# Kernel tuning notes

Measured on AMD Instinct MI355X. Metric: run time of the kernel, lower is better.

## Reference

```python
import jax, jax.numpy as jnp
import numpy as np

N_NODES, N_EDGES, N_EVAL = 100000, 1600000, 200000
IN_C, HID_C, OUT_C = 128, 256, 128


def setup_inputs() -> dict:
    key = jax.random.key(0)
    ks = jax.random.split(key, 10)
    x = jax.random.normal(ks[0], (N_NODES, IN_C), dtype=jnp.float32)
    edge_index = jax.random.randint(ks[1], (2, N_EDGES), 0, N_NODES)
    pos_edge_index = jax.random.randint(ks[2], (2, N_EVAL), 0, N_NODES)
    neg_edge_index = jax.random.randint(ks[3], (2, N_EVAL), 0, N_NODES)

    def glorot(k, fi, fo):
        return jax.random.normal(k, (fi, fo), dtype=jnp.float32) * np.float32(1.0 / np.sqrt(fi))

    W1 = glorot(ks[4], IN_C, HID_C); b1 = jnp.zeros((HID_C,), jnp.float32)
    W2 = glorot(ks[5], HID_C, HID_C); b2 = jnp.zeros((HID_C,), jnp.float32)
    W3 = glorot(ks[6], HID_C, OUT_C); b3 = jnp.zeros((OUT_C,), jnp.float32)
    return dict(x=x, edge_index=edge_index, pos_edge_index=pos_edge_index,
                neg_edge_index=neg_edge_index, W1=W1, b1=b1, W2=W2, b2=b2, W3=W3, b3=b3)


def gcn_layer(x, W, b, src, dst, deg_inv_sqrt):
    # GCNConv: D^{-1/2} (A + I) D^{-1/2} X W + b, degrees include self-loops.
    h = x @ W                                            # [N, F_out]
    norm = deg_inv_sqrt[src] * deg_inv_sqrt[dst]         # [E]
    msg = h[src] * norm[:, None]                          # [E, F_out] gathered messages
    agg = jax.ops.segment_sum(msg, dst, num_segments=x.shape[0])
    agg = agg + h * (deg_inv_sqrt * deg_inv_sqrt)[:, None]  # self-loop contribution
    return agg + b


def reference(x, edge_index, pos_edge_index, neg_edge_index, W1, b1, W2, b2, W3, b3):
    n = x.shape[0]
    src, dst = edge_index[0], edge_index[1]
    # in-degree with self-loops
    deg = jax.ops.segment_sum(jnp.ones_like(dst, dtype=x.dtype), dst, num_segments=n) + 1.0
    dis = jax.lax.rsqrt(deg)
    # encode (index=0); dropout is identity in eval mode
    h = jax.nn.relu(gcn_layer(x, W1, b1, src, dst, dis))
    h = jax.nn.relu(gcn_layer(h, W2, b2, src, dst, dis))
    z = gcn_layer(h, W3, b3, src, dst, dis)
    # decode: per-edge dot product over pos + neg eval edges
    ei = jnp.concatenate([pos_edge_index, neg_edge_index], axis=1)
    logits = jnp.sum(z[ei[0]] * z[ei[1]], axis=-1)
    return logits
```

## Files before the change

### kernel.cpp

```cpp
#include <hip/hip_runtime.h>
#include <cstdint>
#include <cstddef>

#define N_NODES 100000
#define N_EDGES 1600000
#define N_EVAL  200000

typedef __attribute__((ext_vector_type(8))) short bf16x8;
typedef __attribute__((ext_vector_type(4))) float f32x4;
typedef __attribute__((ext_vector_type(8))) unsigned short u16x8;

__device__ __forceinline__ unsigned short f2bf_rne(float f) {
    unsigned int u = __float_as_uint(f);
    unsigned int r = (u + 0x7FFFu + ((u >> 16) & 1u)) >> 16;
    return (unsigned short)r;
}
__device__ __forceinline__ float bf2f(unsigned short h) {
    return __uint_as_float(((unsigned int)h) << 16);
}


__global__ void count_deg_kernel(const int* __restrict__ dst, int* __restrict__ deg, int E) {
    int i = blockIdx.x * blockDim.x + threadIdx.x;
    if (i < E) atomicAdd(&deg[dst[i]], 1);
}

__global__ void dis_kernel(const int* __restrict__ deg, float* __restrict__ dis, int N) {
    int i = blockIdx.x * blockDim.x + threadIdx.x;
    if (i < N) dis[i] = rsqrtf((float)deg[i] + 1.0f);
}

__global__ __launch_bounds__(1024) void scan_kernel(const int* __restrict__ deg,
                                                    int* __restrict__ offsets, int N, int E) {
    __shared__ int sums[1024];
    int t = threadIdx.x;
    int C = (N + 1023) >> 10;
    int lo = t * C;
    int hi = min(lo + C, N);
    int s = 0;
    for (int i = lo; i < hi; ++i) s += deg[i];
    sums[t] = s;
    __syncthreads();
    for (int d = 1; d < 1024; d <<= 1) {
        int add = (t >= d) ? sums[t - d] : 0;
        __syncthreads();
        sums[t] += add;
        __syncthreads();
    }
    int run = sums[t] - s;
    for (int i = lo; i < hi; ++i) { offsets[i] = run; run += deg[i]; }
    if (hi >= N) offsets[N] = E;
}

__global__ void fill_csr_kernel(const int* __restrict__ src, const int* __restrict__ dst,
                                const float* __restrict__ dis, int* __restrict__ cursor,
                                int* __restrict__ csr_src, float* __restrict__ csr_w, int E) {
    int e = blockIdx.x * blockDim.x + threadIdx.x;
    if (e < E) {
        int s = src[e], d = dst[e];
        int p = atomicAdd(&cursor[d], 1);
        csr_src[p] = s;
        csr_w[p] = dis[s] * dis[d];
    }
}


__global__ void wsplit_kernel(const float* __restrict__ W, unsigned short* __restrict__ Wt_hi,
                              unsigned short* __restrict__ Wt_lo, int K, int N) {
    int idx = blockIdx.x * blockDim.x + threadIdx.x;
    if (idx >= K * N) return;
    int k = idx / N, n = idx - k * N;
    float v = W[idx];
    unsigned short h = f2bf_rne(v);
    Wt_hi[(size_t)n * K + k] = h;
    Wt_lo[(size_t)n * K + k] = f2bf_rne(v - bf2f(h));
}


#define KP 40

template <bool BIAS, bool RELU>
__global__ __launch_bounds__(256, 2) void gemm_bf16split_kernel(
    const float* __restrict__ A,
    const unsigned short* __restrict__ Wt_hi,
    const unsigned short* __restrict__ Wt_lo,
    float* __restrict__ C, int M, int N, int K,
    const float* __restrict__ bias)
{
    __shared__ unsigned short As_hi[128][KP];
    __shared__ unsigned short As_lo[128][KP];
    __shared__ unsigned short Bs_hi[128][KP];
    __shared__ unsigned short Bs_lo[128][KP];

    const int tid = threadIdx.x;
    const int m0 = blockIdx.x * 128;
    const int n0 = blockIdx.y * 128;
    const int lane = tid & 63;
    const int wave = tid >> 6;
    const int wm0 = (wave >> 1) * 64;
    const int wn0 = (wave & 1) * 64;
    const int fr = lane & 15;
    const int fk = (lane >> 4) * 8;

    f32x4 acc[4][4];
#pragma unroll
    for (int i = 0; i < 4; ++i)
#pragma unroll
        for (int j = 0; j < 4; ++j) acc[i][j] = (f32x4){0.f, 0.f, 0.f, 0.f};

    const int srow = tid >> 1;
    const int sc0 = (tid & 1) * 16;
    const int agrow = m0 + srow;
    const float* Ap = A + (size_t)agrow * K + sc0;
    const unsigned short* Bh = Wt_hi + (size_t)(n0 + srow) * K + sc0;
    const unsigned short* Bl = Wt_lo + (size_t)(n0 + srow) * K + sc0;

    for (int k0 = 0; k0 < K; k0 += 32) {
        float a[16];
        if (agrow < M) {
            *(float4*)(a)      = *(const float4*)(Ap + k0);
            *(float4*)(a + 4)  = *(const float4*)(Ap + k0 + 4);
            *(float4*)(a + 8)  = *(const float4*)(Ap + k0 + 8);
            *(float4*)(a + 12) = *(const float4*)(Ap + k0 + 12);
        } else {
#pragma unroll
            for (int i = 0; i < 16; ++i) a[i] = 0.f;
        }
        unsigned short h[16], l[16];
#pragma unroll
        for (int i = 0; i < 16; ++i) {
            unsigned short hh = f2bf_rne(a[i]);
            h[i] = hh;
            l[i] = f2bf_rne(a[i] - bf2f(hh));
        }
        *(u16x8*)&As_hi[srow][sc0]     = *(const u16x8*)(h);
        *(u16x8*)&As_hi[srow][sc0 + 8] = *(const u16x8*)(h + 8);
        *(u16x8*)&As_lo[srow][sc0]     = *(const u16x8*)(l);
        *(u16x8*)&As_lo[srow][sc0 + 8] = *(const u16x8*)(l + 8);
        *(u16x8*)&Bs_hi[srow][sc0]     = *(const u16x8*)(Bh + k0);
        *(u16x8*)&Bs_hi[srow][sc0 + 8] = *(const u16x8*)(Bh + k0 + 8);
        *(u16x8*)&Bs_lo[srow][sc0]     = *(const u16x8*)(Bl + k0);
        *(u16x8*)&Bs_lo[srow][sc0 + 8] = *(const u16x8*)(Bl + k0 + 8);
        __syncthreads();

        bf16x8 af_h[4], af_l[4], bf_h[4], bf_l[4];
#pragma unroll
        for (int i = 0; i < 4; ++i) {
            af_h[i] = *(const bf16x8*)&As_hi[wm0 + i * 16 + fr][fk];
            af_l[i] = *(const bf16x8*)&As_lo[wm0 + i * 16 + fr][fk];
            bf_h[i] = *(const bf16x8*)&Bs_hi[wn0 + i * 16 + fr][fk];
            bf_l[i] = *(const bf16x8*)&Bs_lo[wn0 + i * 16 + fr][fk];
        }
#pragma unroll
        for (int i = 0; i < 4; ++i)
#pragma unroll
            for (int j = 0; j < 4; ++j) {
                acc[i][j] = __builtin_amdgcn_mfma_f32_16x16x32_bf16(af_h[i], bf_h[j], acc[i][j], 0, 0, 0);
                acc[i][j] = __builtin_amdgcn_mfma_f32_16x16x32_bf16(af_l[i], bf_h[j], acc[i][j], 0, 0, 0);
                acc[i][j] = __builtin_amdgcn_mfma_f32_16x16x32_bf16(af_h[i], bf_l[j], acc[i][j], 0, 0, 0);
            }
        __syncthreads();
    }

#pragma unroll
    for (int j = 0; j < 4; ++j) {
        const int col = n0 + wn0 + j * 16 + fr;
        const float bb = BIAS ? bias[col] : 0.f;
#pragma unroll
        for (int i = 0; i < 4; ++i) {
            const int rbase = m0 + wm0 + i * 16 + (lane >> 4) * 4;
#pragma unroll
            for (int r = 0; r < 4; ++r) {
                const int row = rbase + r;
                if (row < M) {
                    float v = acc[i][j][r] + bb;
                    if (RELU) v = fmaxf(v, 0.f);
                    C[(size_t)row * N + col] = v;
                }
            }
        }
    }
}


template <int VEC>
__device__ __forceinline__ void vload(float (&r)[VEC], const float* __restrict__ p) {
    if constexpr (VEC == 4) {
        float4 v = *(const float4*)p;
        r[0] = v.x; r[1] = v.y; r[2] = v.z; r[3] = v.w;
    } else {
        float2 v = *(const float2*)p;
        r[0] = v.x; r[1] = v.y;
    }
}

template <int F, bool BIAS, bool RELU>
__global__ __launch_bounds__(256) void aggregate_vec_kernel(
    const float* __restrict__ H,
    const int* __restrict__ offsets,
    const int* __restrict__ csr_src,
    const float* __restrict__ csr_w,
    const float* __restrict__ dis,
    const float* __restrict__ bias,
    float* __restrict__ OUT, int N)
{
    constexpr int VEC = F / 64;
    const int node = blockIdx.x * 4 + (threadIdx.x >> 6);
    if (node >= N) return;
    const int lane = threadIdx.x & 63;
    const int col = lane * VEC;

    const float d = dis[node];
    float acc[VEC];
    {
        float v[VEC];
        vload<VEC>(v, H + (size_t)node * F + col);
        const float dd = d * d;
#pragma unroll
        for (int q = 0; q < VEC; ++q) acc[q] = v[q] * dd;
    }

    const int e0 = offsets[node], e1 = offsets[node + 1];
    int e = e0;
    for (; e + 4 <= e1; e += 4) {
        int s0 = csr_src[e], s1 = csr_src[e + 1], s2 = csr_src[e + 2], s3 = csr_src[e + 3];
        float w0 = csr_w[e], w1 = csr_w[e + 1], w2 = csr_w[e + 2], w3 = csr_w[e + 3];
        float v0[VEC], v1[VEC], v2[VEC], v3[VEC];
        vload<VEC>(v0, H + (size_t)s0 * F + col);
        vload<VEC>(v1, H + (size_t)s1 * F + col);
        vload<VEC>(v2, H + (size_t)s2 * F + col);
        vload<VEC>(v3, H + (size_t)s3 * F + col);
#pragma unroll
        for (int q = 0; q < VEC; ++q) acc[q] = fmaf(w0, v0[q], acc[q]);
#pragma unroll
        for (int q = 0; q < VEC; ++q) acc[q] = fmaf(w1, v1[q], acc[q]);
#pragma unroll
        for (int q = 0; q < VEC; ++q) acc[q] = fmaf(w2, v2[q], acc[q]);
#pragma unroll
        for (int q = 0; q < VEC; ++q) acc[q] = fmaf(w3, v3[q], acc[q]);
    }
    for (; e < e1; ++e) {
        int s0 = csr_src[e];
        float w0 = csr_w[e];
        float v0[VEC];
        vload<VEC>(v0, H + (size_t)s0 * F + col);
#pragma unroll
        for (int q = 0; q < VEC; ++q) acc[q] = fmaf(w0, v0[q], acc[q]);
    }

    if (BIAS) {
        float b[VEC];
        vload<VEC>(b, bias + col);
#pragma unroll
        for (int q = 0; q < VEC; ++q) acc[q] += b[q];
    }
    if (RELU) {
#pragma unroll
        for (int q = 0; q < VEC; ++q) acc[q] = fmaxf(acc[q], 0.f);
    }

    float* op = OUT + (size_t)node * F + col;
    if constexpr (VEC == 4) {
        *(float4*)op = make_float4(acc[0], acc[1], acc[2], acc[3]);
    } else {
        *(float2*)op = make_float2(acc[0], acc[1]);
    }
}


__global__ __launch_bounds__(256) void decode_kernel(const float* __restrict__ z,
                                                     const int* __restrict__ pos,
                                                     const int* __restrict__ neg,
                                                     float* __restrict__ out)
{
    const int wave = threadIdx.x >> 6;
    const int lane = threadIdx.x & 63;
    const int e = blockIdx.x * 4 + wave;
    if (e >= 2 * N_EVAL) return;
    int a, b;
    if (e < N_EVAL) { a = pos[e];          b = pos[N_EVAL + e]; }
    else            { a = neg[e - N_EVAL]; b = neg[e]; }
    const float2 za = *(const float2*)(z + (size_t)a * 128 + lane * 2);
    const float2 zb = *(const float2*)(z + (size_t)b * 128 + lane * 2);
    float v = za.x * zb.x + za.y * zb.y;
#pragma unroll
    for (int d = 32; d > 0; d >>= 1) v += __shfl_xor(v, d);
    if (lane == 0) out[e] = v;
}


extern "C" void kernel_launch(void* const* d_in, const int* in_sizes, int n_in,
                              void* d_out, int out_size, void* d_ws, size_t ws_size,
                              hipStream_t stream)
{
    const float* x  = (const float*)d_in[0];
    const int*   ei = (const int*)d_in[1];
    const int*  pos = (const int*)d_in[2];
    const int*  neg = (const int*)d_in[3];
    const float* W1 = (const float*)d_in[4];
    const float* b1 = (const float*)d_in[5];
    const float* W2 = (const float*)d_in[6];
    const float* b2 = (const float*)d_in[7];
    const float* W3 = (const float*)d_in[8];
    const float* b3 = (const float*)d_in[9];
    float* out = (float*)d_out;

    const int N = N_NODES, E = N_EDGES;

    char* p = (char*)d_ws;
    auto alloc = [&](size_t bytes) {
        char* r = p;
        p += (bytes + 255) & ~(size_t)255;
        return r;
    };
    int*   deg     = (int*)  alloc((size_t)N * 4);
    int*   offsets = (int*)  alloc((size_t)(N + 1) * 4);
    int*   cursor  = (int*)  alloc((size_t)N * 4);
    float* dis     = (float*)alloc((size_t)N * 4);
    int*   csrc    = (int*)  alloc((size_t)E * 4);
    float* cw      = (float*)alloc((size_t)E * 4);
    float* P       = (float*)alloc((size_t)N * 256 * 4);
    float* Q       = (float*)alloc((size_t)N * 256 * 4);
    unsigned short* W1h = (unsigned short*)alloc((size_t)256 * 128 * 2);
    unsigned short* W1l = (unsigned short*)alloc((size_t)256 * 128 * 2);
    unsigned short* W2h = (unsigned short*)alloc((size_t)256 * 256 * 2);
    unsigned short* W2l = (unsigned short*)alloc((size_t)256 * 256 * 2);
    unsigned short* W3h = (unsigned short*)alloc((size_t)128 * 256 * 2);
    unsigned short* W3l = (unsigned short*)alloc((size_t)128 * 256 * 2);

    const int* src = ei;
    const int* dst = ei + E;

    wsplit_kernel<<<(128 * 256 + 255) / 256, 256, 0, stream>>>(W1, W1h, W1l, 128, 256);
    wsplit_kernel<<<(256 * 256 + 255) / 256, 256, 0, stream>>>(W2, W2h, W2l, 256, 256);
    wsplit_kernel<<<(256 * 128 + 255) / 256, 256, 0, stream>>>(W3, W3h, W3l, 256, 128);

    hipMemsetAsync(deg, 0, (size_t)N * 4, stream);
    count_deg_kernel<<<(E + 255) / 256, 256, 0, stream>>>(dst, deg, E);
    dis_kernel<<<(N + 255) / 256, 256, 0, stream>>>(deg, dis, N);
    scan_kernel<<<1, 1024, 0, stream>>>(deg, offsets, N, E);
    hipMemcpyAsync(cursor, offsets, (size_t)N * 4, hipMemcpyDeviceToDevice, stream);
    fill_csr_kernel<<<(E + 255) / 256, 256, 0, stream>>>(src, dst, dis, cursor, csrc, cw, E);

    const int agg_grid = (N + 3) / 4;
    const int mblocks = (N + 127) / 128;

    aggregate_vec_kernel<128, false, false><<<agg_grid, 256, 0, stream>>>(
        x, offsets, csrc, cw, dis, nullptr, P, N);
    gemm_bf16split_kernel<true, true><<<dim3(mblocks, 2), 256, 0, stream>>>(
        P, W1h, W1l, Q, N, 256, 128, b1);

    gemm_bf16split_kernel<false, false><<<dim3(mblocks, 2), 256, 0, stream>>>(
        Q, W2h, W2l, P, N, 256, 256, nullptr);
    aggregate_vec_kernel<256, true, true><<<agg_grid, 256, 0, stream>>>(
        P, offsets, csrc, cw, dis, b2, Q, N);

    gemm_bf16split_kernel<false, false><<<dim3(mblocks, 1), 256, 0, stream>>>(
        Q, W3h, W3l, P, N, 128, 256, nullptr);
    float* Z = Q;
    aggregate_vec_kernel<128, true, false><<<agg_grid, 256, 0, stream>>>(
        P, offsets, csrc, cw, dis, b3, Z, N);

    decode_kernel<<<(2 * N_EVAL + 3) / 4, 256, 0, stream>>>(Z, pos, neg, out);
}
```

Before: 1.057 ms.

## Interleave CSR src/weight pairs, unroll aggregation by 8, batch decode edges per wave

Stores each CSR entry's source index and normalized weight as one int2, so the aggregation kernel issues a single load per edge instead of two separate array loads. The aggregation inner loop is unrolled to 8 edges to keep more independent row gathers in flight, with a 2-edge and 1-edge tail. The decode kernel now handles 4 eval edges per wave, overlapping their gathers and interleaving the shuffle reductions. More registers per thread may reduce occupancy in the F=256 aggregation.

```diff
diff --git a/kernel.cpp b/kernel.cpp
--- a/kernel.cpp
+++ b/kernel.cpp
@@ -54,13 +54,12 @@
 
 __global__ void fill_csr_kernel(const int* __restrict__ src, const int* __restrict__ dst,
                                 const float* __restrict__ dis, int* __restrict__ cursor,
-                                int* __restrict__ csr_src, float* __restrict__ csr_w, int E) {
+                                int2* __restrict__ csr, int E) {
     int e = blockIdx.x * blockDim.x + threadIdx.x;
     if (e < E) {
         int s = src[e], d = dst[e];
         int p = atomicAdd(&cursor[d], 1);
-        csr_src[p] = s;
-        csr_w[p] = dis[s] * dis[d];
+        csr[p] = make_int2(s, __float_as_int(dis[s] * dis[d]));
     }
 }
 
@@ -198,8 +197,7 @@
 __global__ __launch_bounds__(256) void aggregate_vec_kernel(
     const float* __restrict__ H,
     const int* __restrict__ offsets,
-    const int* __restrict__ csr_src,
-    const float* __restrict__ csr_w,
+    const int2* __restrict__ csr,
     const float* __restrict__ dis,
     const float* __restrict__ bias,
     float* __restrict__ OUT, int N)
@@ -222,28 +220,36 @@
 
     const int e0 = offsets[node], e1 = offsets[node + 1];
     int e = e0;
-    for (; e + 4 <= e1; e += 4) {
-        int s0 = csr_src[e], s1 = csr_src[e + 1], s2 = csr_src[e + 2], s3 = csr_src[e + 3];
-        float w0 = csr_w[e], w1 = csr_w[e + 1], w2 = csr_w[e + 2], w3 = csr_w[e + 3];
-        float v0[VEC], v1[VEC], v2[VEC], v3[VEC];
-        vload<VEC>(v0, H + (size_t)s0 * F + col);
-        vload<VEC>(v1, H + (size_t)s1 * F + col);
-        vload<VEC>(v2, H + (size_t)s2 * F + col);
-        vload<VEC>(v3, H + (size_t)s3 * F + col);
+    for (; e + 8 <= e1; e += 8) {
+        int2 c[8];
+#pragma unroll
+        for (int q = 0; q < 8; ++q) c[q] = csr[e + q];
+        float v[8][VEC];
+#pragma unroll
+        for (int q = 0; q < 8; ++q) vload<VEC>(v[q], H + (size_t)c[q].x * F + col);
+#pragma unroll
+        for (int q = 0; q < 8; ++q) {
+            const float w = __int_as_float(c[q].y);
+#pragma unroll
+            for (int vv = 0; vv < VEC; ++vv) acc[vv] = fmaf(w, v[q][vv], acc[vv]);
+        }
+    }
+    for (; e + 2 <= e1; e += 2) {
+        int2 c0 = csr[e], c1 = csr[e + 1];
+        float v0[VEC], v1[VEC];
+        vload<VEC>(v0, H + (size_t)c0.x * F + col);
+        vload<VEC>(v1, H + (size_t)c1.x * F + col);
+        const float w0 = __int_as_float(c0.y), w1 = __int_as_float(c1.y);
 #pragma unroll
         for (int q = 0; q < VEC; ++q) acc[q] = fmaf(w0, v0[q], acc[q]);
 #pragma unroll
         for (int q = 0; q < VEC; ++q) acc[q] = fmaf(w1, v1[q], acc[q]);
-#pragma unroll
-        for (int q = 0; q < VEC; ++q) acc[q] = fmaf(w2, v2[q], acc[q]);
-#pragma unroll
-        for (int q = 0; q < VEC; ++q) acc[q] = fmaf(w3, v3[q], acc[q]);
-    }
-    for (; e < e1; ++e) {
-        int s0 = csr_src[e];
-        float w0 = csr_w[e];
+    }
+    if (e < e1) {
+        int2 c0 = csr[e];
         float v0[VEC];
-        vload<VEC>(v0, H + (size_t)s0 * F + col);
+        vload<VEC>(v0, H + (size_t)c0.x * F + col);
+        const float w0 = __int_as_float(c0.y);
 #pragma unroll
         for (int q = 0; q < VEC; ++q) acc[q] = fmaf(w0, v0[q], acc[q]);
     }
@@ -275,17 +281,33 @@
 {
     const int wave = threadIdx.x >> 6;
     const int lane = threadIdx.x & 63;
-    const int e = blockIdx.x * 4 + wave;
-    if (e >= 2 * N_EVAL) return;
-    int a, b;
-    if (e < N_EVAL) { a = pos[e];          b = pos[N_EVAL + e]; }
-    else            { a = neg[e - N_EVAL]; b = neg[e]; }
-    const float2 za = *(const float2*)(z + (size_t)a * 128 + lane * 2);
-    const float2 zb = *(const float2*)(z + (size_t)b * 128 + lane * 2);
-    float v = za.x * zb.x + za.y * zb.y;
-#pragma unroll
-    for (int d = 32; d > 0; d >>= 1) v += __shfl_xor(v, d);
-    if (lane == 0) out[e] = v;
+    const int ebase = (blockIdx.x * 4 + wave) * 4;
+    if (ebase >= 2 * N_EVAL) return;
+    int ia[4], ib[4];
+#pragma unroll
+    for (int q = 0; q < 4; ++q) {
+        const int e = ebase + q;
+        if (e < N_EVAL) { ia[q] = pos[e];          ib[q] = pos[N_EVAL + e]; }
+        else            { ia[q] = neg[e - N_EVAL]; ib[q] = neg[e]; }
+    }
+    float2 za[4], zb[4];
+#pragma unroll
+    for (int q = 0; q < 4; ++q) {
+        za[q] = *(const float2*)(z + (size_t)ia[q] * 128 + lane * 2);
+        zb[q] = *(const float2*)(z + (size_t)ib[q] * 128 + lane * 2);
+    }
+    float v[4];
+#pragma unroll
+    for (int q = 0; q < 4; ++q) v[q] = za[q].x * zb[q].x + za[q].y * zb[q].y;
+#pragma unroll
+    for (int d = 32; d > 0; d >>= 1) {
+#pragma unroll
+        for (int q = 0; q < 4; ++q) v[q] += __shfl_xor(v[q], d);
+    }
+    if (lane == 0) {
+#pragma unroll
+        for (int q = 0; q < 4; ++q) out[ebase + q] = v[q];
+    }
 }
 
 
@@ -317,8 +339,7 @@
     int*   offsets = (int*)  alloc((size_t)(N + 1) * 4);
     int*   cursor  = (int*)  alloc((size_t)N * 4);
     float* dis     = (float*)alloc((size_t)N * 4);
-    int*   csrc    = (int*)  alloc((size_t)E * 4);
-    float* cw      = (float*)alloc((size_t)E * 4);
+    int2*  csr     = (int2*) alloc((size_t)E * 8);
     float* P       = (float*)alloc((size_t)N * 256 * 4);
     float* Q       = (float*)alloc((size_t)N * 256 * 4);
     unsigned short* W1h = (unsigned short*)alloc((size_t)256 * 128 * 2);
@@ -340,26 +361,26 @@
     dis_kernel<<<(N + 255) / 256, 256, 0, stream>>>(deg, dis, N);
     scan_kernel<<<1, 1024, 0, stream>>>(deg, offsets, N, E);
     hipMemcpyAsync(cursor, offsets, (size_t)N * 4, hipMemcpyDeviceToDevice, stream);
-    fill_csr_kernel<<<(E + 255) / 256, 256, 0, stream>>>(src, dst, dis, cursor, csrc, cw, E);
+    fill_csr_kernel<<<(E + 255) / 256, 256, 0, stream>>>(src, dst, dis, cursor, csr, E);
 
     const int agg_grid = (N + 3) / 4;
     const int mblocks = (N + 127) / 128;
 
     aggregate_vec_kernel<128, false, false><<<agg_grid, 256, 0, stream>>>(
-        x, offsets, csrc, cw, dis, nullptr, P, N);
+        x, offsets, csr, dis, nullptr, P, N);
     gemm_bf16split_kernel<true, true><<<dim3(mblocks, 2), 256, 0, stream>>>(
         P, W1h, W1l, Q, N, 256, 128, b1);
 
     gemm_bf16split_kernel<false, false><<<dim3(mblocks, 2), 256, 0, stream>>>(
         Q, W2h, W2l, P, N, 256, 256, nullptr);
     aggregate_vec_kernel<256, true, true><<<agg_grid, 256, 0, stream>>>(
-        P, offsets, csrc, cw, dis, b2, Q, N);
+        P, offsets, csr, dis, b2, Q, N);
 
     gemm_bf16split_kernel<false, false><<<dim3(mblocks, 1), 256, 0, stream>>>(
         Q, W3h, W3l, P, N, 128, 256, nullptr);
     float* Z = Q;
     aggregate_vec_kernel<128, true, false><<<agg_grid, 256, 0, stream>>>(
-        P, offsets, csrc, cw, dis, b3, Z, N);
-
-    decode_kernel<<<(2 * N_EVAL + 3) / 4, 256, 0, stream>>>(Z, pos, neg, out);
-}
+        P, offsets, csr, dis, b3, Z, N);
+
+    decode_kernel<<<(2 * N_EVAL + 15) / 16, 256, 0, stream>>>(Z, pos, neg, out);
+}
```

Result: faster. 1.005 ms (-5.0%).
